# Kernel optimization log

Hardware: AMD Instinct MI355X
Metric: run time of the kernel (lower is better)

## Reference

```python
import jax, jax.numpy as jnp
import numpy as np

B, T, C = 16, 4096, 256


def setup_inputs() -> dict:
    key = jax.random.key(0)
    kx, kl = jax.random.split(key)
    x = jax.random.normal(kx, (B, T, C), dtype=jnp.float32)
    lengths = jax.random.randint(kl, (B,), T // 2, T + 1)  # valid lengths per sample
    pool_ranges = lengths  # region to pool over; k <= pool_range guaranteed by layer/total_layers choice
    return {
        "x": x,
        "lengths": lengths,
        "pool_ranges": pool_ranges,
        "top_k": 4,
        "layer": 1,
        "total_layers": 4,
    }


def _pool_one(xb, k, pool_range):
    # xb: [T, C]; keep, per column independently, the k largest values among the
    # first pool_range rows, preserving original row order (torch kmax_pooling).
    Trows, Ccols = xb.shape
    valid = jnp.arange(Trows) < pool_range            # [T]
    vals = jnp.where(valid[:, None], xb, -jnp.inf)    # mask invalid rows to rank last
    order = jnp.argsort(-vals, axis=0)                # descending order per column
    rank = jnp.argsort(order, axis=0)                 # inverse permutation = rank of each row
    keep = (rank < k) & valid[:, None]                # [T, C] which entries survive
    pos = jnp.cumsum(keep.astype(jnp.int32), axis=0) - 1  # compacted output row per column
    idx = jnp.where(keep, pos, Trows)                 # dropped entries -> dummy row Trows
    cols = jnp.arange(Ccols)[None, :]
    out = jnp.zeros((Trows + 1, Ccols), xb.dtype).at[idx, cols].set(
        jnp.where(keep, xb, jnp.zeros((), xb.dtype))
    )
    return out[:-1]                                   # [T, C]; rows >= k are zero padding


def reference(x, lengths, pool_ranges, top_k, layer, total_layers):
    # pool_target = max(top_k, ceil((total_layers - layer)/total_layers * length))
    num = total_layers - layer
    k = jnp.maximum(top_k, (num * lengths + total_layers - 1) // total_layers)
    k = jnp.minimum(k, pool_ranges)  # topk requires k <= available rows
    results = jax.vmap(_pool_one)(x, k, pool_ranges)  # [B, T, C], zero-padded past k_i
    pool_result_ranges = k
    return results, pool_result_ranges
```

## Files before the change

kernel.cpp:

```cpp
#include <hip/hip_runtime.h>
#include <stdint.h>


constexpr int T_ROWS = 4096;
constexpr int C_COLS = 256;
constexpr int NBATCH = 16;
constexpr int NSUB   = 4;
constexpr size_t NTOT = (size_t)NBATCH * T_ROWS * C_COLS;

__device__ __forceinline__ int compute_k(const int* lengths, const int* pool_ranges,
                                         const int* p_top_k, const int* p_layer,
                                         const int* p_total, int b, int* pr_out)
{
    int pr = pool_ranges[b];
    pr = pr < 0 ? 0 : (pr > T_ROWS ? T_ROWS : pr);
    const int len   = lengths[b];
    const int top_k = p_top_k[0];
    const int tot   = p_total[0];
    const int num   = tot - p_layer[0];
    int k = (num * len + tot - 1) / tot;
    if (k < top_k) k = top_k;
    if (k > pr)    k = pr;
    *pr_out = pr;
    return k;
}

__global__ __launch_bounds__(256)
void transpose_key_kernel(const float* __restrict__ x, uint32_t* __restrict__ xT)
{
    __shared__ uint32_t tile[64][65];
    const int bid = blockIdx.x;
    const int b   = bid >> 8;
    const int tt  = (bid >> 2) & 63;
    const int ct  = bid & 3;
    const int t0  = tt * 64, c0 = ct * 64;
    const int tid = threadIdx.x;
    const int qq  = tid & 15;
    const int rr  = tid >> 4;

    #pragma unroll
    for (int it = 0; it < 4; ++it) {
        const int r = it * 16 + rr;
        const float4 v = *reinterpret_cast<const float4*>(
            x + ((size_t)(b * T_ROWS + t0 + r) << 8) + c0 + qq * 4);
        const uint32_t w4[4] = {__float_as_uint(v.x), __float_as_uint(v.y),
                                __float_as_uint(v.z), __float_as_uint(v.w)};
        #pragma unroll
        for (int j = 0; j < 4; ++j)
            tile[qq * 4 + j][r] = w4[j] ^ ((w4[j] >> 31) ? 0xFFFFFFFFu : 0x80000000u);
    }
    __syncthreads();
    #pragma unroll
    for (int it = 0; it < 4; ++it) {
        const int cl = it * 16 + rr;
        uint4 o;
        o.x = tile[cl][qq * 4 + 0];
        o.y = tile[cl][qq * 4 + 1];
        o.z = tile[cl][qq * 4 + 2];
        o.w = tile[cl][qq * 4 + 3];
        *reinterpret_cast<uint4*>(
            xT + ((size_t)(b * C_COLS + c0 + cl) << 12) + t0 + qq * 4) = o;
    }
}

__global__ __launch_bounds__(256)
void kmax_select_kernel(const uint32_t* __restrict__ xT,
                        const int* __restrict__ lengths,
                        const int* __restrict__ pool_ranges,
                        const int* __restrict__ p_top_k,
                        const int* __restrict__ p_layer,
                        const int* __restrict__ p_total,
                        float* __restrict__ out,
                        float* __restrict__ ws)
{
    __shared__ uint32_t data_s[4][T_ROWS];
    __shared__ uint32_t hist[4][NSUB][256];

    const int t    = threadIdx.x;
    const int lane = t & 63;
    const int wid  = t >> 6;
    const int bid  = blockIdx.x;
    const int b    = bid >> 6;
    const int cg   = bid & 63;
    const int c    = cg * 4 + wid;

    int pr;
    const int k = compute_k(lengths, pool_ranges, p_top_k, p_layer, p_total, b, &pr);

    const size_t colbase = (size_t)(b * C_COLS + c) << 12;
    const uint4* cp = reinterpret_cast<const uint4*>(xT + colbase) + lane;
    uint32_t* mycol = &data_s[wid][0];
    const int rb = lane * 4;

    {
        uint4 pf[4];
        #pragma unroll
        for (int i = 0; i < 4; ++i) pf[i] = cp[i * 64];
        #pragma unroll
        for (int i = 0; i < 16; ++i) {
            const uint4 v = pf[i & 3];
            if (i + 4 < 16) pf[i & 3] = cp[(i + 4) * 64];
            *reinterpret_cast<uint4*>(&mycol[i * 256 + rb]) = v;
        }
    }

    if (k > 0) {
        uint32_t* hp = &hist[wid][0][0];
        {
            uint4* hz = reinterpret_cast<uint4*>(hp);
            const uint4 z4 = make_uint4(0u, 0u, 0u, 0u);
            #pragma unroll
            for (int z = 0; z < NSUB; ++z) hz[z * 64 + lane] = z4;
        }

        uint32_t prefix = 0u, pmask = 0u, rem = (uint32_t)k;

        #pragma unroll 1
        for (int pass = 0; pass < 4; ++pass) {
            const int shift     = 24 - 8 * pass;
            const int sub_shift = shift ? (shift - 2) : 0;
            #pragma unroll 1
            for (int i = 0; i < 16; ++i) {
                const uint4 v = *reinterpret_cast<const uint4*>(&mycol[i * 256 + rb]);
                const int rowb = i * 256 + rb;
                const uint32_t raw[4] = {v.x, v.y, v.z, v.w};
                #pragma unroll
                for (int j = 0; j < 4; ++j) {
                    const uint32_t ui = raw[j];
                    if ((rowb + j < pr) && ((ui & pmask) == prefix)) {
                        const uint32_t d   = 255u - ((ui >> shift) & 255u);
                        const uint32_t sub = (ui >> sub_shift) & (NSUB - 1u);
                        atomicAdd(&hp[sub * 256u + ((d + 4u * sub) & 255u)], 1u);
                    }
                }
            }
            uint32_t c4[4] = {0u, 0u, 0u, 0u};
            {
                const uint4 z4 = make_uint4(0u, 0u, 0u, 0u);
                #pragma unroll
                for (int s = 0; s < NSUB; ++s) {
                    uint32_t* ap = &hp[s * 256u + ((4u * (uint32_t)lane + 4u * s) & 255u)];
                    const uint4 a = *reinterpret_cast<const uint4*>(ap);
                    *reinterpret_cast<uint4*>(ap) = z4;
                    c4[0] += a.x; c4[1] += a.y; c4[2] += a.z; c4[3] += a.w;
                }
            }
            uint32_t loc[4], ssum = 0;
            #pragma unroll
            for (int q = 0; q < 4; ++q) { loc[q] = ssum; ssum += c4[q]; }
            uint32_t incl = ssum;
            #pragma unroll
            for (int off = 1; off < 64; off <<= 1) {
                const uint32_t nb = __shfl_up(incl, (unsigned)off, 64);
                if (lane >= off) incl += nb;
            }
            const uint32_t gexcl = incl - ssum;
            uint32_t sel = 0, nrem = 0;
            bool found = false;
            #pragma unroll
            for (int q = 0; q < 4; ++q) {
                const uint32_t sbb = gexcl + loc[q];
                if (sbb < rem && sbb + c4[q] >= rem) {
                    sel   = 255u - (uint32_t)(4 * lane + q);
                    nrem  = rem - sbb;
                    found = true;
                }
            }
            const unsigned long long fm = __ballot(found);
            const int src = __ffsll(fm) - 1;
            sel  = __shfl(sel,  src, 64);
            nrem = __shfl(nrem, src, 64);
            prefix |= sel << shift;
            pmask  |= 0xFFu << shift;
            rem = nrem;
        }

        const uint32_t th = prefix, tn = rem;
        uint32_t G = 0, E = 0;
        float* dst = ws + colbase;
        #pragma unroll 1
        for (int i = 0; i < 16; ++i) {
            const uint4 v = *reinterpret_cast<const uint4*>(&mycol[i * 256 + rb]);
            const int rowb = i * 256 + rb;
            const uint32_t raw[4] = {v.x, v.y, v.z, v.w};
            uint32_t gt[4], eq[4], pk = 0, uu[4];
            #pragma unroll
            for (int j = 0; j < 4; ++j) {
                uu[j] = (rowb + j < pr) ? raw[j] : 0u;
                gt[j] = (uu[j] > th) ? 1u : 0u;
                eq[j] = ((rowb + j < pr) && uu[j] == th) ? 1u : 0u;
                pk += (gt[j] << 16) | eq[j];
            }
            uint32_t incl = pk;
            #pragma unroll
            for (int off = 1; off < 64; off <<= 1) {
                const uint32_t nb = __shfl_up(incl, (unsigned)off, 64);
                if (lane >= off) incl += nb;
            }
            const uint32_t tot  = __shfl(incl, 63, 64);
            const uint32_t base = incl - pk;
            uint32_t g = G + (base >> 16), e = E + (base & 0xFFFFu);
            #pragma unroll
            for (int j = 0; j < 4; ++j) {
                if (gt[j] || (eq[j] && e < tn)) {
                    const uint32_t pos  = g + (e < tn ? e : tn);
                    const uint32_t bits = uu[j] ^ ((uu[j] >> 31) ? 0x80000000u
                                                                 : 0xFFFFFFFFu);
                    dst[pos] = __uint_as_float(bits);
                }
                g += gt[j];
                e += eq[j];
            }
            G += tot >> 16;
            E += tot & 0xFFFFu;
        }
    }

    if (cg == 0 && t == 0)
        out[NTOT + (size_t)b] = (float)k;
}

__global__ __launch_bounds__(256)
void finalize_kernel(const float* __restrict__ ws,
                     const int* __restrict__ lengths,
                     const int* __restrict__ pool_ranges,
                     const int* __restrict__ p_top_k,
                     const int* __restrict__ p_layer,
                     const int* __restrict__ p_total,
                     float* __restrict__ out)
{
    __shared__ float tile[64][65];
    const int bid  = blockIdx.x;
    const int b    = bid >> 8;
    const int pt   = (bid >> 2) & 63;
    const int ct   = bid & 3;
    const int pos0 = pt * 64, c0 = ct * 64;

    int pr;
    const int k = compute_k(lengths, pool_ranges, p_top_k, p_layer, p_total, b, &pr);

    const int tid = threadIdx.x;
    const int qq  = tid & 15;
    const int rr  = tid >> 4;
    float4* out4 = reinterpret_cast<float4*>(out);
    const float4 z4 = make_float4(0.f, 0.f, 0.f, 0.f);

    if (pos0 < k) {
        const float4* ws4 = reinterpret_cast<const float4*>(ws);
        #pragma unroll
        for (int it = 0; it < 4; ++it) {
            const int cl = it * 16 + rr;
            const float4 v = ws4[((size_t)(b * C_COLS + c0 + cl) << 10)
                                 + (pos0 >> 2) + qq];
            tile[cl][qq * 4 + 0] = v.x;
            tile[cl][qq * 4 + 1] = v.y;
            tile[cl][qq * 4 + 2] = v.z;
            tile[cl][qq * 4 + 3] = v.w;
        }
        __syncthreads();
        #pragma unroll
        for (int it = 0; it < 4; ++it) {
            const int r = it * 16 + rr;
            float4 v;
            v.x = tile[qq * 4 + 0][r];
            v.y = tile[qq * 4 + 1][r];
            v.z = tile[qq * 4 + 2][r];
            v.w = tile[qq * 4 + 3][r];
            if (pos0 + r >= k) v = z4;
            out4[((size_t)(b * T_ROWS + pos0 + r) << 6) + (c0 >> 2) + qq] = v;
        }
    } else {
        #pragma unroll
        for (int it = 0; it < 4; ++it) {
            const int r = it * 16 + rr;
            out4[((size_t)(b * T_ROWS + pos0 + r) << 6) + (c0 >> 2) + qq] = z4;
        }
    }
}

extern "C" void kernel_launch(void* const* d_in, const int* in_sizes, int n_in,
                              void* d_out, int out_size, void* d_ws, size_t ws_size,
                              hipStream_t stream)
{
    const float* x            = (const float*)d_in[0];
    const int*   lengths      = (const int*)d_in[1];
    const int*   pool_ranges  = (const int*)d_in[2];
    const int*   top_k        = (const int*)d_in[3];
    const int*   layer        = (const int*)d_in[4];
    const int*   total_layers = (const int*)d_in[5];
    float*       out          = (float*)d_out;
    float*       ws           = (float*)d_ws;

    hipLaunchKernelGGL(transpose_key_kernel, dim3(4096), dim3(256), 0, stream,
                       x, (uint32_t*)ws);
    hipLaunchKernelGGL(kmax_select_kernel, dim3(1024), dim3(256), 0, stream,
                       (const uint32_t*)ws, lengths, pool_ranges,
                       top_k, layer, total_layers, out, ws);
    hipLaunchKernelGGL(finalize_kernel, dim3(4096), dim3(256), 0, stream,
                       ws, lengths, pool_ranges, top_k, layer, total_layers, out);
}
```

Measured before the change: 102.3 us.

## Fuse first histogram pass into load, swizzle LDS layout, single-scan compaction

Builds the first radix-select histogram pass during the global-to-LDS column load instead of in a separate sweep. Stores each column in LDS with an XOR swizzle so each lane can own a contiguous 64-row chunk without bank conflicts. The compaction stage then does one per-lane count, one wave prefix scan and one scatter pass, replacing the 16 per-chunk shuffle scans. In exchange, each lane's output writes become strided and less coalesced, and the swizzle adds index arithmetic.

```diff
diff --git a/kernel.cpp b/kernel.cpp
--- a/kernel.cpp
+++ b/kernel.cpp
@@ -89,8 +89,15 @@
 
     const size_t colbase = (size_t)(b * C_COLS + c) << 12;
     const uint4* cp = reinterpret_cast<const uint4*>(xT + colbase) + lane;
-    uint32_t* mycol = &data_s[wid][0];
-    const int rb = lane * 4;
+    uint4* mycol4 = reinterpret_cast<uint4*>(&data_s[wid][0]);
+    uint32_t* hp = &hist[wid][0][0];
+
+    {
+        uint4* hz = reinterpret_cast<uint4*>(hp);
+        const uint4 z4 = make_uint4(0u, 0u, 0u, 0u);
+        #pragma unroll
+        for (int z = 0; z < NSUB; ++z) hz[z * 64 + lane] = z4;
+    }
 
     {
         uint4 pf[4];
@@ -100,37 +107,47 @@
         for (int i = 0; i < 16; ++i) {
             const uint4 v = pf[i & 3];
             if (i + 4 < 16) pf[i & 3] = cp[(i + 4) * 64];
-            *reinterpret_cast<uint4*>(&mycol[i * 256 + rb]) = v;
+            const int phys = i * 64 + (lane & 48)
+                           + ((lane & 15) ^ ((i * 4 + (lane >> 4)) & 15));
+            mycol4[phys] = v;
+            if (k > 0) {
+                const int rowb = i * 256 + lane * 4;
+                const uint32_t raw[4] = {v.x, v.y, v.z, v.w};
+                #pragma unroll
+                for (int j = 0; j < 4; ++j) {
+                    if (rowb + j < pr) {
+                        const uint32_t ui  = raw[j];
+                        const uint32_t d   = 255u - (ui >> 24);
+                        const uint32_t sub = (ui >> 22) & (NSUB - 1u);
+                        atomicAdd(&hp[sub * 256u + ((d + 4u * sub) & 255u)], 1u);
+                    }
+                }
+            }
         }
     }
 
     if (k > 0) {
-        uint32_t* hp = &hist[wid][0][0];
-        {
-            uint4* hz = reinterpret_cast<uint4*>(hp);
-            const uint4 z4 = make_uint4(0u, 0u, 0u, 0u);
-            #pragma unroll
-            for (int z = 0; z < NSUB; ++z) hz[z * 64 + lane] = z4;
-        }
-
         uint32_t prefix = 0u, pmask = 0u, rem = (uint32_t)k;
 
         #pragma unroll 1
         for (int pass = 0; pass < 4; ++pass) {
             const int shift     = 24 - 8 * pass;
             const int sub_shift = shift ? (shift - 2) : 0;
-            #pragma unroll 1
-            for (int i = 0; i < 16; ++i) {
-                const uint4 v = *reinterpret_cast<const uint4*>(&mycol[i * 256 + rb]);
-                const int rowb = i * 256 + rb;
-                const uint32_t raw[4] = {v.x, v.y, v.z, v.w};
-                #pragma unroll
-                for (int j = 0; j < 4; ++j) {
-                    const uint32_t ui = raw[j];
-                    if ((rowb + j < pr) && ((ui & pmask) == prefix)) {
-                        const uint32_t d   = 255u - ((ui >> shift) & 255u);
-                        const uint32_t sub = (ui >> sub_shift) & (NSUB - 1u);
-                        atomicAdd(&hp[sub * 256u + ((d + 4u * sub) & 255u)], 1u);
+            if (pass > 0) {
+                #pragma unroll 4
+                for (int s = 0; s < 16; ++s) {
+                    const int phys = lane * 16 + (s ^ (lane & 15));
+                    const uint4 v = mycol4[phys];
+                    const int rowb = lane * 64 + s * 4;
+                    const uint32_t raw[4] = {v.x, v.y, v.z, v.w};
+                    #pragma unroll
+                    for (int j = 0; j < 4; ++j) {
+                        const uint32_t ui = raw[j];
+                        if ((rowb + j < pr) && ((ui & pmask) == prefix)) {
+                            const uint32_t d   = 255u - ((ui >> shift) & 255u);
+                            const uint32_t sub = (ui >> sub_shift) & (NSUB - 1u);
+                            atomicAdd(&hp[sub * 256u + ((d + 4u * sub) & 255u)], 1u);
+                        }
                     }
                 }
             }
@@ -176,43 +193,54 @@
         }
 
         const uint32_t th = prefix, tn = rem;
-        uint32_t G = 0, E = 0;
+        uint32_t gcnt = 0, ecnt = 0;
+        #pragma unroll 4
+        for (int s = 0; s < 16; ++s) {
+            const int phys = lane * 16 + (s ^ (lane & 15));
+            const uint4 v = mycol4[phys];
+            const int rowb = lane * 64 + s * 4;
+            const uint32_t raw[4] = {v.x, v.y, v.z, v.w};
+            #pragma unroll
+            for (int j = 0; j < 4; ++j) {
+                if (rowb + j < pr) {
+                    gcnt += (raw[j] > th) ? 1u : 0u;
+                    ecnt += (raw[j] == th) ? 1u : 0u;
+                }
+            }
+        }
+        const uint32_t pk = (gcnt << 16) | ecnt;
+        uint32_t incl = pk;
+        #pragma unroll
+        for (int off = 1; off < 64; off <<= 1) {
+            const uint32_t nb = __shfl_up(incl, (unsigned)off, 64);
+            if (lane >= off) incl += nb;
+        }
+        const uint32_t excl = incl - pk;
+        uint32_t g = excl >> 16, e = excl & 0xFFFFu;
+
         float* dst = ws + colbase;
-        #pragma unroll 1
-        for (int i = 0; i < 16; ++i) {
-            const uint4 v = *reinterpret_cast<const uint4*>(&mycol[i * 256 + rb]);
-            const int rowb = i * 256 + rb;
+        #pragma unroll 4
+        for (int s = 0; s < 16; ++s) {
+            const int phys = lane * 16 + (s ^ (lane & 15));
+            const uint4 v = mycol4[phys];
+            const int rowb = lane * 64 + s * 4;
             const uint32_t raw[4] = {v.x, v.y, v.z, v.w};
-            uint32_t gt[4], eq[4], pk = 0, uu[4];
             #pragma unroll
             for (int j = 0; j < 4; ++j) {
-                uu[j] = (rowb + j < pr) ? raw[j] : 0u;
-                gt[j] = (uu[j] > th) ? 1u : 0u;
-                eq[j] = ((rowb + j < pr) && uu[j] == th) ? 1u : 0u;
-                pk += (gt[j] << 16) | eq[j];
-            }
-            uint32_t incl = pk;
-            #pragma unroll
-            for (int off = 1; off < 64; off <<= 1) {
-                const uint32_t nb = __shfl_up(incl, (unsigned)off, 64);
-                if (lane >= off) incl += nb;
-            }
-            const uint32_t tot  = __shfl(incl, 63, 64);
-            const uint32_t base = incl - pk;
-            uint32_t g = G + (base >> 16), e = E + (base & 0xFFFFu);
-            #pragma unroll
-            for (int j = 0; j < 4; ++j) {
-                if (gt[j] || (eq[j] && e < tn)) {
-                    const uint32_t pos  = g + (e < tn ? e : tn);
-                    const uint32_t bits = uu[j] ^ ((uu[j] >> 31) ? 0x80000000u
-                                                                 : 0xFFFFFFFFu);
-                    dst[pos] = __uint_as_float(bits);
-                }
-                g += gt[j];
-                e += eq[j];
-            }
-            G += tot >> 16;
-            E += tot & 0xFFFFu;
+                if (rowb + j < pr) {
+                    const uint32_t ui   = raw[j];
+                    const bool     isgt = ui > th;
+                    const bool     iseq = (ui == th);
+                    if (isgt || (iseq && e < tn)) {
+                        const uint32_t pos  = g + (e < tn ? e : tn);
+                        const uint32_t bits = ui ^ ((ui >> 31) ? 0x80000000u
+                                                               : 0xFFFFFFFFu);
+                        dst[pos] = __uint_as_float(bits);
+                    }
+                    g += isgt ? 1u : 0u;
+                    e += iseq ? 1u : 0u;
+                }
+            }
         }
     }
 
```

New measurement: 125.8 us. 23.1% more time.
